# Kernel optimization log

Measured on AMD Instinct MI355X. Metric: run time of the kernel, lower is better.

Reference implementation:

```python
import jax, jax.numpy as jnp
import numpy as np

TOP_K = 2
TEMP = 1.0  # router_temperature
B, L, D, F, DF, DR, DH, E = 32, 256, 256, 8, 64, 256, 512, 8
DIN = D + DF  # expert/router input: concat(hidden, feat_emb)


def setup_inputs() -> dict:
    key = jax.random.key(0)
    ks = jax.random.split(key, 12)
    gn = lambda k, shape, fan: jax.random.normal(k, shape, dtype=jnp.float32) * (fan ** -0.5)
    return {
        "hidden": jax.random.normal(ks[0], (B, L, D), dtype=jnp.float32),
        "feat": jax.random.uniform(ks[1], (B, L, F), dtype=jnp.float32),
        "W_feat": gn(ks[2], (F, DF), F),
        "b_feat": jnp.zeros((DF,), jnp.float32),
        "Wr1": gn(ks[3], (DIN, DR), DIN),
        "br1": jnp.zeros((DR,), jnp.float32),
        "Wr2": gn(ks[4], (DR, E), DR),
        "br2": jnp.zeros((E,), jnp.float32),
        "We1": gn(ks[5], (E, DIN, DH), DIN),
        "be1": jnp.zeros((E, DH), jnp.float32),
        "We2": gn(ks[6], (E, DH, D), DH),
        "be2": jnp.zeros((E, D), jnp.float32),
    }


def reference(hidden, feat, W_feat, b_feat, Wr1, br1, Wr2, br2, We1, be1, We2, be2):
    # feature embedding
    feat_emb = feat @ W_feat + b_feat                       # [B,L,DF]
    x = jnp.concatenate([hidden, feat_emb], axis=-1)        # [B,L,DIN]

    # token-level learned router with temperature + top-k gating
    hr = jax.nn.gelu(x @ Wr1 + br1)                         # [B,L,DR]
    gate_logits = (hr @ Wr2 + br2) / TEMP                   # [B,L,E]
    topv, topi = jax.lax.top_k(gate_logits, TOP_K)          # [B,L,K]
    w = jax.nn.softmax(topv, axis=-1)                       # renormalized over top-k
    gate_weights = (jax.nn.one_hot(topi, E, dtype=w.dtype) * w[..., None]).sum(-2)  # [B,L,E]

    # experts: per-expert 2-layer MLP (dense compute, sparse combine via gates)
    he = jax.nn.gelu(jnp.einsum('bli,eih->bleh', x, We1) + be1)   # [B,L,E,DH]
    eo = jnp.einsum('bleh,eho->bleo', he, We2) + be2              # [B,L,E,D]
    stage_delta = jnp.einsum('ble,bleo->blo', gate_weights, eo)   # next_hidden - hidden

    return stage_delta, gate_weights, gate_logits
```

## Files before the change

### kernel.cpp

```cpp
#include <hip/hip_runtime.h>
#include <hip/hip_bf16.h>

#define N_TOK   8192
#define DMODEL  256
#define NFEAT   8
#define DFEAT   64
#define DIN     320
#define DRTR    256
#define NE      8
#define DH      512
#define TE      32
#define RTB     32
#define FIXCAP  128
#define FIXTHR  2e-3f

#define OUT_GATEW  (N_TOK*DMODEL)
#define OUT_LOGITS (N_TOK*DMODEL + N_TOK*NE)

typedef short v8s __attribute__((ext_vector_type(8)));
typedef float v4f __attribute__((ext_vector_type(4)));

__device__ __forceinline__ unsigned short f2bf(float f){
  unsigned u = __float_as_uint(f);
  return (unsigned short)((u + 0x7FFFu + ((u>>16)&1u)) >> 16);
}
__device__ __forceinline__ float bf2f(unsigned short h){
  return __uint_as_float(((unsigned)h)<<16);
}
__device__ __forceinline__ float gelu_tanh(float v){
  float u = 0.7978845608028654f * (v + 0.044715f * v * v * v);
  float a = fabsf(u);
  float e = __expf(-2.0f * a);
  float t = (1.0f - e) / (1.0f + e);
  t = copysignf(t, u);
  return 0.5f * v * (1.0f + t);
}

__global__ void k_init(int* __restrict__ cnts, int* __restrict__ nfix){
  if (threadIdx.x < NE) cnts[threadIdx.x] = 0;
  if (threadIdx.x == NE) *nfix = 0;
}

__global__ __launch_bounds__(256) void k_prep1(const float* __restrict__ W,
                                               unsigned short* __restrict__ dh,
                                               unsigned short* __restrict__ dl){
  int gid = blockIdx.x*256 + threadIdx.x;
  int l = gid & 63; int w = gid >> 6;
  int nt = w & 31; w >>= 5; int kstep = w % 10; int e = w / 10;
  int n = nt*16 + (l&15);
  int kb = kstep*32 + ((l>>4)<<3);
  const float* src = W + ((size_t)e*DIN + kb)*DH + n;
  unsigned short hs[8], ls[8];
  #pragma unroll
  for (int i=0;i<8;i++){
    float v = src[(size_t)i*DH];
    unsigned short h = f2bf(v);
    hs[i] = h; ls[i] = f2bf(v - bf2f(h));
  }
  size_t off = (size_t)gid*8;
  *(v8s*)(dh+off) = *(v8s*)hs;
  *(v8s*)(dl+off) = *(v8s*)ls;
}

__global__ __launch_bounds__(256) void k_prep2(const float* __restrict__ W,
                                               unsigned short* __restrict__ dh,
                                               unsigned short* __restrict__ dl){
  int gid = blockIdx.x*256 + threadIdx.x;
  int l = gid & 63; int w = gid >> 6;
  int nt = w & 15; w >>= 4; int kstep = w & 15; int e = w >> 4;
  int n = nt*16 + (l&15);
  int kb = kstep*32 + ((l>>4)<<3);
  const float* src = W + ((size_t)e*DH + kb)*DMODEL + n;
  unsigned short hs[8], ls[8];
  #pragma unroll
  for (int i=0;i<8;i++){
    float v = src[(size_t)i*DMODEL];
    unsigned short h = f2bf(v);
    hs[i] = h; ls[i] = f2bf(v - bf2f(h));
  }
  size_t off = (size_t)gid*8;
  *(v8s*)(dh+off) = *(v8s*)hs;
  *(v8s*)(dl+off) = *(v8s*)ls;
}

__global__ __launch_bounds__(256) void k_prepr(const float* __restrict__ W,
                                               unsigned short* __restrict__ dh,
                                               unsigned short* __restrict__ dl){
  int gid = blockIdx.x*256 + threadIdx.x;
  if (gid >= 10240) return;
  int l = gid & 63; int w = gid >> 6;
  int nt = w & 15; int kstep = w >> 4;
  int n = nt*16 + (l&15);
  int kb = kstep*32 + ((l>>4)<<3);
  const float* src = W + (size_t)kb*DRTR + n;
  unsigned short hs[8], ls[8];
  #pragma unroll
  for (int i=0;i<8;i++){
    float v = src[(size_t)i*DRTR];
    unsigned short h = f2bf(v);
    hs[i] = h; ls[i] = f2bf(v - bf2f(h));
  }
  size_t off = (size_t)gid*8;
  *(v8s*)(dh+off) = *(v8s*)hs;
  *(v8s*)(dl+off) = *(v8s*)ls;
}

#define MM6(c0,c1,ah0,ah1,al0,al1,bh,bl) do{ \
  c0 = __builtin_amdgcn_mfma_f32_16x16x32_bf16(ah0, bh, c0, 0,0,0); \
  c1 = __builtin_amdgcn_mfma_f32_16x16x32_bf16(ah1, bh, c1, 0,0,0); \
  c0 = __builtin_amdgcn_mfma_f32_16x16x32_bf16(al0, bh, c0, 0,0,0); \
  c1 = __builtin_amdgcn_mfma_f32_16x16x32_bf16(al1, bh, c1, 0,0,0); \
  c0 = __builtin_amdgcn_mfma_f32_16x16x32_bf16(ah0, bl, c0, 0,0,0); \
  c1 = __builtin_amdgcn_mfma_f32_16x16x32_bf16(ah1, bl, c1, 0,0,0); }while(0)

#define XLOFF  10496
#define HELOFF 16640

__global__ __launch_bounds__(512) void k_rmfma(
    const float* __restrict__ hidden, const float* __restrict__ feat,
    const float* __restrict__ Wf, const float* __restrict__ bfe,
    const unsigned short* __restrict__ Wr1h, const unsigned short* __restrict__ Wr1l,
    const float* __restrict__ br1,
    const float* __restrict__ Wr2, const float* __restrict__ br2,
    float* __restrict__ out,
    int* __restrict__ cnts, unsigned* __restrict__ lists, float* __restrict__ topw,
    int* __restrict__ nfix, int* __restrict__ fixlist)
{
  __shared__ unsigned short sm[21248];
  __shared__ float part_lds[512];
  __shared__ float lg_lds[RTB*NE];
  float* hrf = (float*)sm;
  const int tid = threadIdx.x;
  const int t0 = blockIdx.x * RTB;

  {
    float4 z = make_float4(0.f,0.f,0.f,0.f);
    float4* dst = ((float4*)out) + (size_t)blockIdx.x*2048 + tid;
    #pragma unroll
    for (int r=0;r<4;r++) dst[r*512] = z;
  }
  #pragma unroll
  for (int r=0;r<4;r++){
    int idx = r*512 + tid; int t = idx >> 6, lane = idx & 63;
    float4 h4 = ((const float4*)(hidden + (size_t)(t0+t)*DMODEL))[lane];
    unsigned short h0=f2bf(h4.x),h1=f2bf(h4.y),h2=f2bf(h4.z),h3=f2bf(h4.w);
    unsigned short l0=f2bf(h4.x-bf2f(h0)),l1=f2bf(h4.y-bf2f(h1)),
                   l2=f2bf(h4.z-bf2f(h2)),l3=f2bf(h4.w-bf2f(h3));
    uint2 hp, lp;
    hp.x=(unsigned)h0|((unsigned)h1<<16); hp.y=(unsigned)h2|((unsigned)h3<<16);
    lp.x=(unsigned)l0|((unsigned)l1<<16); lp.y=(unsigned)l2|((unsigned)l3<<16);
    *(uint2*)&sm[t*328 + lane*4]         = hp;
    *(uint2*)&sm[XLOFF + t*328 + lane*4] = lp;
  }
  #pragma unroll
  for (int r=0;r<4;r++){
    int idx = r*512 + tid; int t = idx >> 6, j = idx & 63;
    float acc = bfe[j];
    #pragma unroll
    for (int f=0; f<NFEAT; f++) acc += feat[(size_t)(t0+t)*NFEAT + f] * Wf[f*DFEAT + j];
    unsigned short h = f2bf(acc);
    sm[t*328 + DMODEL + j]         = h;
    sm[XLOFF + t*328 + DMODEL + j] = f2bf(acc - bf2f(h));
  }
  __syncthreads();

  const int wv = tid >> 6;
  const int l  = tid & 63;
  const int lg = l >> 4;
  const int lr = l & 15;

  v4f acc[2][2];
  {
    v4f z = {0.f,0.f,0.f,0.f};
    acc[0][0]=z; acc[0][1]=z; acc[1][0]=z; acc[1][1]=z;
    v8s bh_a[2], bl_a[2], bh_b[2], bl_b[2];
    auto ldBr = [&](int ks, v8s (&bh)[2], v8s (&bl)[2]){
      #pragma unroll
      for (int j=0;j<2;++j){
        size_t boff = ((size_t)(ks*16 + wv*2 + j)*64 + l)*8;
        bh[j] = *(const v8s*)(Wr1h + boff);
        bl[j] = *(const v8s*)(Wr1l + boff);
      }
    };
    ldBr(0, bh_a, bl_a);
    for (int ks=0; ks<10; ks+=2){
      v8s ah0 = *(const v8s*)&sm[( 0+lr)*328 + ks*32 + lg*8];
      v8s ah1 = *(const v8s*)&sm[(16+lr)*328 + ks*32 + lg*8];
      v8s al0 = *(const v8s*)&sm[XLOFF + ( 0+lr)*328 + ks*32 + lg*8];
      v8s al1 = *(const v8s*)&sm[XLOFF + (16+lr)*328 + ks*32 + lg*8];
      ldBr(ks+1, bh_b, bl_b);
      #pragma unroll
      for (int j=0;j<2;++j) MM6(acc[0][j],acc[1][j], ah0,ah1,al0,al1, bh_a[j],bl_a[j]);
      v8s ch0 = *(const v8s*)&sm[( 0+lr)*328 + (ks+1)*32 + lg*8];
      v8s ch1 = *(const v8s*)&sm[(16+lr)*328 + (ks+1)*32 + lg*8];
      v8s cl0 = *(const v8s*)&sm[XLOFF + ( 0+lr)*328 + (ks+1)*32 + lg*8];
      v8s cl1 = *(const v8s*)&sm[XLOFF + (16+lr)*328 + (ks+1)*32 + lg*8];
      if (ks+2<10) ldBr(ks+2, bh_a, bl_a);
      #pragma unroll
      for (int j=0;j<2;++j) MM6(acc[0][j],acc[1][j], ch0,ch1,cl0,cl1, bh_b[j],bl_b[j]);
    }
  }
  __syncthreads();
  #pragma unroll
  for (int j=0;j<2;++j){
    int col = (wv*2+j)*16 + lr;
    float b1 = br1[col];
    #pragma unroll
    for (int m=0;m<2;m++)
      #pragma unroll
      for (int r=0;r<4;r++){
        int row = m*16 + lg*4 + r;
        hrf[row*264 + col] = gelu_tanh(acc[m][j][r] + b1);
      }
  }
  __syncthreads();
  {
    int q = tid >> 8, rr = tid & 255, t = rr >> 3, e = rr & 7;
    float a0=0.f,a1=0.f,a2=0.f,a3=0.f;
    #pragma unroll 4
    for (int k4=0;k4<32;k4++){
      float4 h4 = ((const float4*)hrf)[t*66 + q*32 + k4];
      int row = q*128 + k4*4;
      a0 += h4.x * Wr2[(row+0)*NE + e];
      a1 += h4.y * Wr2[(row+1)*NE + e];
      a2 += h4.z * Wr2[(row+2)*NE + e];
      a3 += h4.w * Wr2[(row+3)*NE + e];
    }
    part_lds[tid] = (a0+a1)+(a2+a3);
  }
  __syncthreads();
  if (tid < RTB*NE){
    int t = tid >> 3, e = tid & 7;
    float lgv = br2[e] + part_lds[tid] + part_lds[tid+256];
    out[OUT_LOGITS + (size_t)(t0+t)*NE + e] = lgv;
    lg_lds[t*NE + e] = lgv;
  }
  __syncthreads();
  if (tid < RTB){
    int t = tid, tok = t0 + t;
    float v1=-3.4e38f, v2=-3.4e38f, v3=-3.4e38f; int i1=-1, i2=-1;
    #pragma unroll
    for (int e=0;e<NE;e++){
      float v = lg_lds[t*NE+e];
      if (v > v1){ v3=v2; v2=v1; i2=i1; v1=v; i1=e; }
      else if (v > v2){ v3=v2; v2=v; i2=e; }
      else if (v > v3){ v3=v; }
    }
    bool defer = false;
    if (v2 - v3 < FIXTHR){
      int fi = atomicAdd(nfix, 1);
      if (fi < FIXCAP){ fixlist[fi] = tok; defer = true; }
    }
    if (!defer){
      float d   = expf(v2 - v1);
      float inv = 1.0f/(1.0f + d);
      float w1 = inv, w2 = d*inv;
      #pragma unroll
      for (int e=0;e<NE;e++){
        float gv = (e==i1) ? w1 : ((e==i2) ? w2 : 0.f);
        out[OUT_GATEW + (size_t)tok*NE + e] = gv;
      }
      int p1 = atomicAdd(&cnts[i1], 1);
      lists[i1*N_TOK + p1] = (unsigned)(tok<<1);
      int p2 = atomicAdd(&cnts[i2], 1);
      lists[i2*N_TOK + p2] = (unsigned)((tok<<1) | 1);
      topw[tok*2]   = w1;
      topw[tok*2+1] = w2;
    }
  }
}

__global__ __launch_bounds__(256) void k_fix(
    const float* __restrict__ hidden, const float* __restrict__ feat,
    const float* __restrict__ Wf, const float* __restrict__ bfe,
    const float* __restrict__ Wr1, const float* __restrict__ br1,
    const float* __restrict__ Wr2, const float* __restrict__ br2,
    float* __restrict__ out, const int* __restrict__ nfix, const int* __restrict__ fixlist)
{
  int nf = *nfix; if (nf > FIXCAP) nf = FIXCAP;
  if ((int)blockIdx.x >= nf) return;
  const int tok = fixlist[blockIdx.x];
  const int tid = threadIdx.x;
  __shared__ float xf[DIN];
  __shared__ float hr[DRTR];
  if (tid < DMODEL) xf[tid] = hidden[(size_t)tok*DMODEL + tid];
  if (tid < DFEAT){
    float acc = bfe[tid];
    #pragma unroll
    for (int f=0; f<NFEAT; f++) acc += feat[(size_t)tok*NFEAT + f] * Wf[f*DFEAT + tid];
    xf[DMODEL + tid] = acc;
  }
  __syncthreads();
  {
    float acc = br1[tid];
    for (int i=0;i<DIN;i++) acc += xf[i] * Wr1[(size_t)i*DRTR + tid];
    hr[tid] = gelu_tanh(acc);
  }
  __syncthreads();
  if (tid < NE){
    float acc = br2[tid];
    for (int i=0;i<DRTR;i++) acc += hr[i] * Wr2[i*NE + tid];
    out[OUT_LOGITS + (size_t)tok*NE + tid] = acc;
  }
}

__global__ void k_gatefix(float* __restrict__ out,
                          int* __restrict__ cnts, unsigned* __restrict__ lists,
                          float* __restrict__ topw,
                          const int* __restrict__ nfix, const int* __restrict__ fixlist)
{
  int nf = *nfix; if (nf > FIXCAP) nf = FIXCAP;
  int i = threadIdx.x;
  if (i >= nf) return;
  int tok = fixlist[i];
  float v1=-3.4e38f, v2=-3.4e38f; int i1=-1, i2=-1;
  #pragma unroll
  for (int e=0;e<NE;e++){
    float v = out[OUT_LOGITS + (size_t)tok*NE + e];
    if (v > v1){ v2=v1; i2=i1; v1=v; i1=e; }
    else if (v > v2){ v2=v; i2=e; }
  }
  float d   = expf(v2 - v1);
  float inv = 1.0f/(1.0f + d);
  float w1 = inv, w2 = d*inv;
  #pragma unroll
  for (int e=0;e<NE;e++){
    float gv = (e==i1) ? w1 : ((e==i2) ? w2 : 0.f);
    out[OUT_GATEW + (size_t)tok*NE + e] = gv;
  }
  int p1 = atomicAdd(&cnts[i1], 1);
  lists[i1*N_TOK + p1] = (unsigned)(tok<<1);
  int p2 = atomicAdd(&cnts[i2], 1);
  lists[i2*N_TOK + p2] = (unsigned)((tok<<1) | 1);
  topw[tok*2]   = w1;
  topw[tok*2+1] = w2;
}

__global__ __launch_bounds__(512) void k_expert(
    const float* __restrict__ hidden, const float* __restrict__ feat,
    const float* __restrict__ Wf, const float* __restrict__ bfe,
    const int* __restrict__ cnts, const unsigned* __restrict__ lists,
    const float* __restrict__ topw,
    const unsigned short* __restrict__ W1h, const unsigned short* __restrict__ W1l,
    const unsigned short* __restrict__ W2h, const unsigned short* __restrict__ W2l,
    const float* __restrict__ be1, const float* __restrict__ be2,
    float* __restrict__ out)
{
  __shared__ unsigned short sm[33280];
  __shared__ int   tok_lds[TE];
  __shared__ float w_lds[TE];

  const int e    = blockIdx.x & 7;
  const int tile = blockIdx.x >> 3;
  const int cnt  = cnts[e];
  const int start = tile * TE;
  if (start >= cnt) return;
  const int ntk = min(TE, cnt - start);
  const int tid = threadIdx.x;

  if (tid < TE){
    if (tid < ntk){
      unsigned ent = lists[e*N_TOK + start + tid];
      int tok = (int)(ent >> 1);
      tok_lds[tid] = tok;
      w_lds[tid]   = topw[tok*2 + (ent & 1)];
    } else { tok_lds[tid] = -1; w_lds[tid] = 0.f; }
  }
  __syncthreads();
  #pragma unroll
  for (int r=0;r<4;r++){
    int idx = r*512 + tid; int t = idx >> 6, lane = idx & 63;
    int tok = tok_lds[t];
    float4 h4 = make_float4(0.f,0.f,0.f,0.f);
    if (tok >= 0) h4 = ((const float4*)(hidden + (size_t)tok*DMODEL))[lane];
    unsigned short h0=f2bf(h4.x),h1=f2bf(h4.y),h2=f2bf(h4.z),h3=f2bf(h4.w);
    unsigned short l0=f2bf(h4.x-bf2f(h0)),l1=f2bf(h4.y-bf2f(h1)),
                   l2=f2bf(h4.z-bf2f(h2)),l3=f2bf(h4.w-bf2f(h3));
    uint2 hp, lp;
    hp.x=(unsigned)h0|((unsigned)h1<<16); hp.y=(unsigned)h2|((unsigned)h3<<16);
    lp.x=(unsigned)l0|((unsigned)l1<<16); lp.y=(unsigned)l2|((unsigned)l3<<16);
    *(uint2*)&sm[t*328 + lane*4]         = hp;
    *(uint2*)&sm[XLOFF + t*328 + lane*4] = lp;
  }
  #pragma unroll
  for (int r=0;r<4;r++){
    int idx = r*512 + tid; int t = idx >> 6, j = idx & 63;
    int tok = tok_lds[t];
    float acc = 0.f;
    if (tok >= 0){
      acc = bfe[j];
      #pragma unroll
      for (int f=0; f<NFEAT; f++) acc += feat[(size_t)tok*NFEAT + f] * Wf[f*DFEAT + j];
    }
    unsigned short h = f2bf(acc);
    sm[t*328 + DMODEL + j]         = h;
    sm[XLOFF + t*328 + DMODEL + j] = f2bf(acc - bf2f(h));
  }
  __syncthreads();

  const int wv = tid >> 6;
  const int l  = tid & 63;
  const int lg = l >> 4;
  const int lr = l & 15;

  v4f acc1[2][4];
  {
    v4f z = {0.f,0.f,0.f,0.f};
    #pragma unroll
    for (int m=0;m<2;m++)
      #pragma unroll
      for (int j=0;j<4;j++) acc1[m][j] = z;
    const unsigned short* p1h = W1h + (size_t)e*163840;
    const unsigned short* p1l = W1l + (size_t)e*163840;
    auto ldB1 = [&](int ks, int jh, v8s (&bh)[2], v8s (&bl)[2]){
      #pragma unroll
      for (int j=0;j<2;++j){
        size_t boff = ((size_t)(ks*32 + wv*4 + jh*2 + j)*64 + l)*8;
        bh[j] = *(const v8s*)(p1h + boff);
        bl[j] = *(const v8s*)(p1l + boff);
      }
    };
    v8s bh_a[2], bl_a[2], bh_b[2], bl_b[2];
    ldB1(0,0,bh_a,bl_a);
    for (int ks=0; ks<10; ++ks){
      v8s ah0 = *(const v8s*)&sm[( 0+lr)*328 + ks*32 + lg*8];
      v8s ah1 = *(const v8s*)&sm[(16+lr)*328 + ks*32 + lg*8];
      v8s al0 = *(const v8s*)&sm[XLOFF + ( 0+lr)*328 + ks*32 + lg*8];
      v8s al1 = *(const v8s*)&sm[XLOFF + (16+lr)*328 + ks*32 + lg*8];
      ldB1(ks,1,bh_b,bl_b);
      #pragma unroll
      for (int j=0;j<2;++j) MM6(acc1[0][j],acc1[1][j], ah0,ah1,al0,al1, bh_a[j],bl_a[j]);
      if (ks<9) ldB1(ks+1,0,bh_a,bl_a);
      #pragma unroll
      for (int j=0;j<2;++j) MM6(acc1[0][2+j],acc1[1][2+j], ah0,ah1,al0,al1, bh_b[j],bl_b[j]);
    }
  }
  __syncthreads();
  #pragma unroll
  for (int j=0;j<4;++j){
    int col = (wv*4+j)*16 + lr;
    float b1 = be1[e*DH + col];
    #pragma unroll
    for (int m=0;m<2;m++)
      #pragma unroll
      for (int r=0;r<4;r++){
        float v = gelu_tanh(acc1[m][j][r] + b1);
        int row = m*16 + lg*4 + r;
        unsigned short h = f2bf(v);
        sm[row*520 + col]          = h;
        sm[HELOFF + row*520 + col] = f2bf(v - bf2f(h));
      }
  }
  __syncthreads();
  v4f acc2[2][2];
  {
    v4f z = {0.f,0.f,0.f,0.f};
    acc2[0][0]=z; acc2[0][1]=z; acc2[1][0]=z; acc2[1][1]=z;
    const unsigned short* p2h = W2h + (size_t)e*131072;
    const unsigned short* p2l = W2l + (size_t)e*131072;
    auto ldB2 = [&](int ks, v8s (&bh)[2], v8s (&bl)[2]){
      #pragma unroll
      for (int j=0;j<2;++j){
        size_t boff = ((size_t)(ks*16 + wv*2 + j)*64 + l)*8;
        bh[j] = *(const v8s*)(p2h + boff);
        bl[j] = *(const v8s*)(p2l + boff);
      }
    };
    v8s bh_a[2], bl_a[2], bh_b[2], bl_b[2];
    ldB2(0,bh_a,bl_a);
    for (int ks=0; ks<16; ks+=2){
      v8s ah0 = *(const v8s*)&sm[( 0+lr)*520 + ks*32 + lg*8];
      v8s ah1 = *(const v8s*)&sm[(16+lr)*520 + ks*32 + lg*8];
      v8s al0 = *(const v8s*)&sm[HELOFF + ( 0+lr)*520 + ks*32 + lg*8];
      v8s al1 = *(const v8s*)&sm[HELOFF + (16+lr)*520 + ks*32 + lg*8];
      ldB2(ks+1, bh_b, bl_b);
      #pragma unroll
      for (int j=0;j<2;++j) MM6(acc2[0][j],acc2[1][j], ah0,ah1,al0,al1, bh_a[j],bl_a[j]);
      v8s ch0 = *(const v8s*)&sm[( 0+lr)*520 + (ks+1)*32 + lg*8];
      v8s ch1 = *(const v8s*)&sm[(16+lr)*520 + (ks+1)*32 + lg*8];
      v8s cl0 = *(const v8s*)&sm[HELOFF + ( 0+lr)*520 + (ks+1)*32 + lg*8];
      v8s cl1 = *(const v8s*)&sm[HELOFF + (16+lr)*520 + (ks+1)*32 + lg*8];
      if (ks+2<16) ldB2(ks+2, bh_a, bl_a);
      #pragma unroll
      for (int j=0;j<2;++j) MM6(acc2[0][j],acc2[1][j], ch0,ch1,cl0,cl1, bh_b[j],bl_b[j]);
    }
  }
  #pragma unroll
  for (int j=0;j<2;++j){
    int col = (wv*2+j)*16 + lr;
    float b2 = be2[e*DMODEL + col];
    #pragma unroll
    for (int m=0;m<2;m++)
      #pragma unroll
      for (int r=0;r<4;r++){
        int row = m*16 + lg*4 + r;
        if (row < ntk){
          float w = w_lds[row];
          atomicAdd(out + (size_t)tok_lds[row]*DMODEL + col,
                    w*(acc2[m][j][r] + b2));
        }
      }
  }
}

extern "C" void kernel_launch(void* const* d_in, const int* in_sizes, int n_in,
                              void* d_out, int out_size, void* d_ws, size_t ws_size,
                              hipStream_t stream)
{
  (void)in_sizes; (void)n_in; (void)out_size; (void)ws_size;
  const float* hidden = (const float*)d_in[0];
  const float* feat   = (const float*)d_in[1];
  const float* Wf     = (const float*)d_in[2];
  const float* bfe    = (const float*)d_in[3];
  const float* Wr1    = (const float*)d_in[4];
  const float* br1    = (const float*)d_in[5];
  const float* Wr2    = (const float*)d_in[6];
  const float* br2    = (const float*)d_in[7];
  const float* We1    = (const float*)d_in[8];
  const float* be1    = (const float*)d_in[9];
  const float* We2    = (const float*)d_in[10];
  const float* be2    = (const float*)d_in[11];
  float* out = (float*)d_out;

  char* ws = (char*)d_ws;
  int*      cnts    = (int*)ws;
  int*      nfix    = (int*)(ws + 64);
  int*      fixlist = (int*)(ws + 128);
  unsigned* lists   = (unsigned*)(ws + 1024);
  float*    topw    = (float*)(ws + 263168);
  unsigned short* W1h  = (unsigned short*)(ws + 328704);
  unsigned short* W1l  = (unsigned short*)(ws + 2950144);
  unsigned short* W2h  = (unsigned short*)(ws + 5571584);
  unsigned short* W2l  = (unsigned short*)(ws + 7668736);
  unsigned short* Wr1h = (unsigned short*)(ws + 9765888);
  unsigned short* Wr1l = (unsigned short*)(ws + 9929728);

  hipLaunchKernelGGL(k_init, dim3(1), dim3(64), 0, stream, cnts, nfix);
  hipLaunchKernelGGL(k_prep1, dim3(640), dim3(256), 0, stream, We1, W1h, W1l);
  hipLaunchKernelGGL(k_prep2, dim3(512), dim3(256), 0, stream, We2, W2h, W2l);
  hipLaunchKernelGGL(k_prepr, dim3(40),  dim3(256), 0, stream, Wr1, Wr1h, Wr1l);
  hipLaunchKernelGGL(k_rmfma, dim3(N_TOK/RTB), dim3(512), 0, stream,
                     hidden, feat, Wf, bfe, Wr1h, Wr1l, br1, Wr2, br2,
                     out, cnts, lists, topw, nfix, fixlist);
  hipLaunchKernelGGL(k_fix, dim3(FIXCAP), dim3(256), 0, stream,
                     hidden, feat, Wf, bfe, Wr1, br1, Wr2, br2, out, nfix, fixlist);
  hipLaunchKernelGGL(k_gatefix, dim3(1), dim3(FIXCAP), 0, stream,
                     out, cnts, lists, topw, nfix, fixlist);
  hipLaunchKernelGGL(k_expert, dim3((N_TOK/TE)*NE), dim3(512), 0, stream,
                     hidden, feat, Wf, bfe, cnts, lists, topw,
                     W1h, W1l, W2h, W2l, be1, be2, out);
}
```

Before: 293.8 us.

## Fuse weight prep kernels, stage through LDS, use fragment-ordered LDS layout in experts

Merges the init kernel and the three weight-split prep kernels into one launch. Each block now loads a contiguous weight tile into LDS with coalesced float4 reads before writing the hi/lo bf16 fragments. The expert kernel stores activations and the GELU hidden layer in LDS directly in MFMA fragment order, so A-operand reads become contiguous and need no padding. It also issues the first weight prefetches earlier and adds sched_barriers to pin the order of loads and MFMAs. The cost is more complex index math, and the scheduling barriers may keep the compiler from interleaving instructions well.

```diff
diff --git a/kernel.cpp b/kernel.cpp
--- a/kernel.cpp
+++ b/kernel.cpp
@@ -36,73 +36,84 @@
   return 0.5f * v * (1.0f + t);
 }
 
-__global__ void k_init(int* __restrict__ cnts, int* __restrict__ nfix){
-  if (threadIdx.x < NE) cnts[threadIdx.x] = 0;
-  if (threadIdx.x == NE) *nfix = 0;
-}
-
-__global__ __launch_bounds__(256) void k_prep1(const float* __restrict__ W,
-                                               unsigned short* __restrict__ dh,
-                                               unsigned short* __restrict__ dl){
-  int gid = blockIdx.x*256 + threadIdx.x;
-  int l = gid & 63; int w = gid >> 6;
-  int nt = w & 31; w >>= 5; int kstep = w % 10; int e = w / 10;
-  int n = nt*16 + (l&15);
-  int kb = kstep*32 + ((l>>4)<<3);
-  const float* src = W + ((size_t)e*DIN + kb)*DH + n;
-  unsigned short hs[8], ls[8];
-  #pragma unroll
-  for (int i=0;i<8;i++){
-    float v = src[(size_t)i*DH];
-    unsigned short h = f2bf(v);
-    hs[i] = h; ls[i] = f2bf(v - bf2f(h));
-  }
-  size_t off = (size_t)gid*8;
-  *(v8s*)(dh+off) = *(v8s*)hs;
-  *(v8s*)(dl+off) = *(v8s*)ls;
-}
-
-__global__ __launch_bounds__(256) void k_prep2(const float* __restrict__ W,
-                                               unsigned short* __restrict__ dh,
-                                               unsigned short* __restrict__ dl){
-  int gid = blockIdx.x*256 + threadIdx.x;
-  int l = gid & 63; int w = gid >> 6;
-  int nt = w & 15; w >>= 4; int kstep = w & 15; int e = w >> 4;
-  int n = nt*16 + (l&15);
-  int kb = kstep*32 + ((l>>4)<<3);
-  const float* src = W + ((size_t)e*DH + kb)*DMODEL + n;
-  unsigned short hs[8], ls[8];
-  #pragma unroll
-  for (int i=0;i<8;i++){
-    float v = src[(size_t)i*DMODEL];
-    unsigned short h = f2bf(v);
-    hs[i] = h; ls[i] = f2bf(v - bf2f(h));
-  }
-  size_t off = (size_t)gid*8;
-  *(v8s*)(dh+off) = *(v8s*)hs;
-  *(v8s*)(dl+off) = *(v8s*)ls;
-}
-
-__global__ __launch_bounds__(256) void k_prepr(const float* __restrict__ W,
-                                               unsigned short* __restrict__ dh,
-                                               unsigned short* __restrict__ dl){
-  int gid = blockIdx.x*256 + threadIdx.x;
-  if (gid >= 10240) return;
-  int l = gid & 63; int w = gid >> 6;
-  int nt = w & 15; int kstep = w >> 4;
-  int n = nt*16 + (l&15);
-  int kb = kstep*32 + ((l>>4)<<3);
-  const float* src = W + (size_t)kb*DRTR + n;
-  unsigned short hs[8], ls[8];
-  #pragma unroll
-  for (int i=0;i<8;i++){
-    float v = src[(size_t)i*DRTR];
-    unsigned short h = f2bf(v);
-    hs[i] = h; ls[i] = f2bf(v - bf2f(h));
-  }
-  size_t off = (size_t)gid*8;
-  *(v8s*)(dh+off) = *(v8s*)hs;
-  *(v8s*)(dl+off) = *(v8s*)ls;
+__global__ __launch_bounds__(256) void k_prep(
+    const float* __restrict__ We1, const float* __restrict__ We2,
+    const float* __restrict__ Wr1,
+    unsigned short* __restrict__ W1h, unsigned short* __restrict__ W1l,
+    unsigned short* __restrict__ W2h, unsigned short* __restrict__ W2l,
+    unsigned short* __restrict__ Wr1h, unsigned short* __restrict__ Wr1l,
+    int* __restrict__ cnts, int* __restrict__ nfix)
+{
+  __shared__ float lds[16384];
+  const int b = blockIdx.x;
+  const int tid = threadIdx.x;
+  if (b < 80){
+    int e = b/10, kstep = b%10;
+    const float* src = We1 + ((size_t)e*DIN + kstep*32)*DH;
+    #pragma unroll
+    for (int r=0;r<16;r++) ((float4*)lds)[r*256+tid] = ((const float4*)src)[r*256+tid];
+    __syncthreads();
+    #pragma unroll
+    for (int r=0;r<8;r++){
+      int ent = r*256+tid; int nt = ent>>6, l = ent&63;
+      int n = nt*16 + (l&15); int k0 = (l>>4)*8;
+      unsigned short hs[8], ls[8];
+      #pragma unroll
+      for (int i=0;i<8;i++){
+        float v = lds[(k0+i)*DH + n];
+        unsigned short h = f2bf(v);
+        hs[i]=h; ls[i]=f2bf(v - bf2f(h));
+      }
+      size_t gid = ((size_t)(e*10+kstep)*32 + nt)*64 + l;
+      *(v8s*)(W1h+gid*8) = *(v8s*)hs;
+      *(v8s*)(W1l+gid*8) = *(v8s*)ls;
+    }
+  } else if (b < 208){
+    int e = (b-80)/16, kstep = (b-80)%16;
+    const float* src = We2 + ((size_t)e*DH + kstep*32)*DMODEL;
+    #pragma unroll
+    for (int r=0;r<8;r++) ((float4*)lds)[r*256+tid] = ((const float4*)src)[r*256+tid];
+    __syncthreads();
+    #pragma unroll
+    for (int r=0;r<4;r++){
+      int ent = r*256+tid; int nt = ent>>6, l = ent&63;
+      int n = nt*16 + (l&15); int k0 = (l>>4)*8;
+      unsigned short hs[8], ls[8];
+      #pragma unroll
+      for (int i=0;i<8;i++){
+        float v = lds[(k0+i)*DMODEL + n];
+        unsigned short h = f2bf(v);
+        hs[i]=h; ls[i]=f2bf(v - bf2f(h));
+      }
+      size_t gid = ((size_t)(e*16+kstep)*16 + nt)*64 + l;
+      *(v8s*)(W2h+gid*8) = *(v8s*)hs;
+      *(v8s*)(W2l+gid*8) = *(v8s*)ls;
+    }
+  } else if (b < 218){
+    int kstep = b-208;
+    const float* src = Wr1 + (size_t)kstep*32*DRTR;
+    #pragma unroll
+    for (int r=0;r<8;r++) ((float4*)lds)[r*256+tid] = ((const float4*)src)[r*256+tid];
+    __syncthreads();
+    #pragma unroll
+    for (int r=0;r<4;r++){
+      int ent = r*256+tid; int nt = ent>>6, l = ent&63;
+      int n = nt*16 + (l&15); int k0 = (l>>4)*8;
+      unsigned short hs[8], ls[8];
+      #pragma unroll
+      for (int i=0;i<8;i++){
+        float v = lds[(k0+i)*DRTR + n];
+        unsigned short h = f2bf(v);
+        hs[i]=h; ls[i]=f2bf(v - bf2f(h));
+      }
+      size_t gid = ((size_t)kstep*16 + nt)*64 + l;
+      *(v8s*)(Wr1h+gid*8) = *(v8s*)hs;
+      *(v8s*)(Wr1l+gid*8) = *(v8s*)ls;
+    }
+  } else {
+    if (tid < NE) cnts[tid] = 0;
+    if (tid == NE) *nfix = 0;
+  }
 }
 
 #define MM6(c0,c1,ah0,ah1,al0,al1,bh,bl) do{ \
@@ -114,7 +125,6 @@
   c1 = __builtin_amdgcn_mfma_f32_16x16x32_bf16(ah1, bl, c1, 0,0,0); }while(0)
 
 #define XLOFF  10496
-#define HELOFF 16640
 
 __global__ __launch_bounds__(512) void k_rmfma(
     const float* __restrict__ hidden, const float* __restrict__ feat,
@@ -189,6 +199,7 @@
       v8s al0 = *(const v8s*)&sm[XLOFF + ( 0+lr)*328 + ks*32 + lg*8];
       v8s al1 = *(const v8s*)&sm[XLOFF + (16+lr)*328 + ks*32 + lg*8];
       ldBr(ks+1, bh_b, bl_b);
+      __builtin_amdgcn_sched_barrier(0);
       #pragma unroll
       for (int j=0;j<2;++j) MM6(acc[0][j],acc[1][j], ah0,ah1,al0,al1, bh_a[j],bl_a[j]);
       v8s ch0 = *(const v8s*)&sm[( 0+lr)*328 + (ks+1)*32 + lg*8];
@@ -196,6 +207,7 @@
       v8s cl0 = *(const v8s*)&sm[XLOFF + ( 0+lr)*328 + (ks+1)*32 + lg*8];
       v8s cl1 = *(const v8s*)&sm[XLOFF + (16+lr)*328 + (ks+1)*32 + lg*8];
       if (ks+2<10) ldBr(ks+2, bh_a, bl_a);
+      __builtin_amdgcn_sched_barrier(0);
       #pragma unroll
       for (int j=0;j<2;++j) MM6(acc[0][j],acc[1][j], ch0,ch1,cl0,cl1, bh_b[j],bl_b[j]);
     }
@@ -336,6 +348,8 @@
   topw[tok*2+1] = w2;
 }
 
+#define XFL  10240
+#define HFL  16384
 __global__ __launch_bounds__(512) void k_expert(
     const float* __restrict__ hidden, const float* __restrict__ feat,
     const float* __restrict__ Wf, const float* __restrict__ bfe,
@@ -346,7 +360,7 @@
     const float* __restrict__ be1, const float* __restrict__ be2,
     float* __restrict__ out)
 {
-  __shared__ unsigned short sm[33280];
+  __shared__ unsigned short sm[32768];
   __shared__ int   tok_lds[TE];
   __shared__ float w_lds[TE];
 
@@ -357,6 +371,24 @@
   if (start >= cnt) return;
   const int ntk = min(TE, cnt - start);
   const int tid = threadIdx.x;
+  const int wv = tid >> 6;
+  const int l  = tid & 63;
+  const int lg = l >> 4;
+  const int lr = l & 15;
+
+  const unsigned short* p1h = W1h + (size_t)e*163840;
+  const unsigned short* p1l = W1l + (size_t)e*163840;
+
+  v8s bh_a[2], bl_a[2], bh_b[2], bl_b[2];
+  auto ldB1 = [&](int ks, int jh, v8s (&bh)[2], v8s (&bl)[2]){
+    #pragma unroll
+    for (int j=0;j<2;++j){
+      size_t boff = ((size_t)(ks*32 + wv*4 + jh*2 + j)*64 + l)*8;
+      bh[j] = *(const v8s*)(p1h + boff);
+      bl[j] = *(const v8s*)(p1l + boff);
+    }
+  };
+  ldB1(0,0,bh_a,bl_a);
 
   if (tid < TE){
     if (tid < ntk){
@@ -368,40 +400,44 @@
   }
   __syncthreads();
   #pragma unroll
-  for (int r=0;r<4;r++){
-    int idx = r*512 + tid; int t = idx >> 6, lane = idx & 63;
-    int tok = tok_lds[t];
-    float4 h4 = make_float4(0.f,0.f,0.f,0.f);
-    if (tok >= 0) h4 = ((const float4*)(hidden + (size_t)tok*DMODEL))[lane];
-    unsigned short h0=f2bf(h4.x),h1=f2bf(h4.y),h2=f2bf(h4.z),h3=f2bf(h4.w);
-    unsigned short l0=f2bf(h4.x-bf2f(h0)),l1=f2bf(h4.y-bf2f(h1)),
-                   l2=f2bf(h4.z-bf2f(h2)),l3=f2bf(h4.w-bf2f(h3));
-    uint2 hp, lp;
-    hp.x=(unsigned)h0|((unsigned)h1<<16); hp.y=(unsigned)h2|((unsigned)h3<<16);
-    lp.x=(unsigned)l0|((unsigned)l1<<16); lp.y=(unsigned)l2|((unsigned)l3<<16);
-    *(uint2*)&sm[t*328 + lane*4]         = hp;
-    *(uint2*)&sm[XLOFF + t*328 + lane*4] = lp;
-  }
-  #pragma unroll
-  for (int r=0;r<4;r++){
-    int idx = r*512 + tid; int t = idx >> 6, j = idx & 63;
-    int tok = tok_lds[t];
-    float acc = 0.f;
-    if (tok >= 0){
-      acc = bfe[j];
-      #pragma unroll
-      for (int f=0; f<NFEAT; f++) acc += feat[(size_t)tok*NFEAT + f] * Wf[f*DFEAT + j];
-    }
-    unsigned short h = f2bf(acc);
-    sm[t*328 + DMODEL + j]         = h;
-    sm[XLOFF + t*328 + DMODEL + j] = f2bf(acc - bf2f(h));
-  }
-  __syncthreads();
-
-  const int wv = tid >> 6;
-  const int l  = tid & 63;
-  const int lg = l >> 4;
-  const int lr = l & 15;
+  for (int r=0;r<3;r++){
+    int idx = r*512 + tid;
+    if (idx < 1280){
+      int le = idx & 63; int rest = idx >> 6;
+      int m = rest & 1, ks = rest >> 1;
+      int t = m*16 + (le & 15);
+      int kb = ks*32 + (le >> 4)*8;
+      int tok = tok_lds[t];
+      float v[8];
+      if (tok < 0){
+        #pragma unroll
+        for (int i=0;i<8;i++) v[i] = 0.f;
+      } else if (kb < DMODEL){
+        float4 a = *(const float4*)(hidden + (size_t)tok*DMODEL + kb);
+        float4 b = *(const float4*)(hidden + (size_t)tok*DMODEL + kb + 4);
+        v[0]=a.x; v[1]=a.y; v[2]=a.z; v[3]=a.w;
+        v[4]=b.x; v[5]=b.y; v[6]=b.z; v[7]=b.w;
+      } else {
+        int j0 = kb - DMODEL;
+        #pragma unroll
+        for (int i=0;i<8;i++){
+          float acc = bfe[j0+i];
+          #pragma unroll
+          for (int f=0; f<NFEAT; f++) acc += feat[(size_t)tok*NFEAT + f] * Wf[f*DFEAT + j0+i];
+          v[i] = acc;
+        }
+      }
+      unsigned short hs[8], ls[8];
+      #pragma unroll
+      for (int i=0;i<8;i++){
+        unsigned short h = f2bf(v[i]);
+        hs[i]=h; ls[i]=f2bf(v[i]-bf2f(h));
+      }
+      *(v8s*)&sm[idx*8]       = *(v8s*)hs;
+      *(v8s*)&sm[XFL + idx*8] = *(v8s*)ls;
+    }
+  }
+  __syncthreads();
 
   v4f acc1[2][4];
   {
@@ -410,45 +446,51 @@
     for (int m=0;m<2;m++)
       #pragma unroll
       for (int j=0;j<4;j++) acc1[m][j] = z;
-    const unsigned short* p1h = W1h + (size_t)e*163840;
-    const unsigned short* p1l = W1l + (size_t)e*163840;
-    auto ldB1 = [&](int ks, int jh, v8s (&bh)[2], v8s (&bl)[2]){
-      #pragma unroll
-      for (int j=0;j<2;++j){
-        size_t boff = ((size_t)(ks*32 + wv*4 + jh*2 + j)*64 + l)*8;
-        bh[j] = *(const v8s*)(p1h + boff);
-        bl[j] = *(const v8s*)(p1l + boff);
-      }
-    };
-    v8s bh_a[2], bl_a[2], bh_b[2], bl_b[2];
-    ldB1(0,0,bh_a,bl_a);
     for (int ks=0; ks<10; ++ks){
-      v8s ah0 = *(const v8s*)&sm[( 0+lr)*328 + ks*32 + lg*8];
-      v8s ah1 = *(const v8s*)&sm[(16+lr)*328 + ks*32 + lg*8];
-      v8s al0 = *(const v8s*)&sm[XLOFF + ( 0+lr)*328 + ks*32 + lg*8];
-      v8s al1 = *(const v8s*)&sm[XLOFF + (16+lr)*328 + ks*32 + lg*8];
+      v8s ah0 = *(const v8s*)&sm[((ks*2+0)*64 + l)*8];
+      v8s ah1 = *(const v8s*)&sm[((ks*2+1)*64 + l)*8];
+      v8s al0 = *(const v8s*)&sm[XFL + ((ks*2+0)*64 + l)*8];
+      v8s al1 = *(const v8s*)&sm[XFL + ((ks*2+1)*64 + l)*8];
       ldB1(ks,1,bh_b,bl_b);
+      __builtin_amdgcn_sched_barrier(0);
       #pragma unroll
       for (int j=0;j<2;++j) MM6(acc1[0][j],acc1[1][j], ah0,ah1,al0,al1, bh_a[j],bl_a[j]);
       if (ks<9) ldB1(ks+1,0,bh_a,bl_a);
+      __builtin_amdgcn_sched_barrier(0);
       #pragma unroll
       for (int j=0;j<2;++j) MM6(acc1[0][2+j],acc1[1][2+j], ah0,ah1,al0,al1, bh_b[j],bl_b[j]);
     }
   }
+  const unsigned short* p2h = W2h + (size_t)e*131072;
+  const unsigned short* p2l = W2l + (size_t)e*131072;
+  v8s ch_a[2], cl_a[2], ch_b[2], cl_b[2];
+  auto ldB2 = [&](int ks, v8s (&bh)[2], v8s (&bl)[2]){
+    #pragma unroll
+    for (int j=0;j<2;++j){
+      size_t boff = ((size_t)(ks*16 + wv*2 + j)*64 + l)*8;
+      bh[j] = *(const v8s*)(p2h + boff);
+      bl[j] = *(const v8s*)(p2l + boff);
+    }
+  };
+  ldB2(0, ch_a, cl_a);
   __syncthreads();
   #pragma unroll
   for (int j=0;j<4;++j){
-    int col = (wv*4+j)*16 + lr;
+    int W = wv*4 + j;
+    int col = W*16 + lr;
     float b1 = be1[e*DH + col];
+    int ks2 = W >> 1;
+    int lg2 = (W*2 + (lr>>3)) & 3;
+    int i   = lr & 7;
     #pragma unroll
     for (int m=0;m<2;m++)
       #pragma unroll
       for (int r=0;r<4;r++){
         float v = gelu_tanh(acc1[m][j][r] + b1);
-        int row = m*16 + lg*4 + r;
         unsigned short h = f2bf(v);
-        sm[row*520 + col]          = h;
-        sm[HELOFF + row*520 + col] = f2bf(v - bf2f(h));
+        int dst = ((ks2*2 + m)*64 + lg2*16 + lg*4 + r)*8 + i;
+        sm[dst]       = h;
+        sm[HFL + dst] = f2bf(v - bf2f(h));
       }
   }
   __syncthreads();
@@ -456,33 +498,23 @@
   {
     v4f z = {0.f,0.f,0.f,0.f};
     acc2[0][0]=z; acc2[0][1]=z; acc2[1][0]=z; acc2[1][1]=z;
-    const unsigned short* p2h = W2h + (size_t)e*131072;
-    const unsigned short* p2l = W2l + (size_t)e*131072;
-    auto ldB2 = [&](int ks, v8s (&bh)[2], v8s (&bl)[2]){
-      #pragma unroll
-      for (int j=0;j<2;++j){
-        size_t boff = ((size_t)(ks*16 + wv*2 + j)*64 + l)*8;
-        bh[j] = *(const v8s*)(p2h + boff);
-        bl[j] = *(const v8s*)(p2l + boff);
-      }
-    };
-    v8s bh_a[2], bl_a[2], bh_b[2], bl_b[2];
-    ldB2(0,bh_a,bl_a);
     for (int ks=0; ks<16; ks+=2){
-      v8s ah0 = *(const v8s*)&sm[( 0+lr)*520 + ks*32 + lg*8];
-      v8s ah1 = *(const v8s*)&sm[(16+lr)*520 + ks*32 + lg*8];
-      v8s al0 = *(const v8s*)&sm[HELOFF + ( 0+lr)*520 + ks*32 + lg*8];
-      v8s al1 = *(const v8s*)&sm[HELOFF + (16+lr)*520 + ks*32 + lg*8];
-      ldB2(ks+1, bh_b, bl_b);
-      #pragma unroll
-      for (int j=0;j<2;++j) MM6(acc2[0][j],acc2[1][j], ah0,ah1,al0,al1, bh_a[j],bl_a[j]);
-      v8s ch0 = *(const v8s*)&sm[( 0+lr)*520 + (ks+1)*32 + lg*8];
-      v8s ch1 = *(const v8s*)&sm[(16+lr)*520 + (ks+1)*32 + lg*8];
-      v8s cl0 = *(const v8s*)&sm[HELOFF + ( 0+lr)*520 + (ks+1)*32 + lg*8];
-      v8s cl1 = *(const v8s*)&sm[HELOFF + (16+lr)*520 + (ks+1)*32 + lg*8];
-      if (ks+2<16) ldB2(ks+2, bh_a, bl_a);
-      #pragma unroll
-      for (int j=0;j<2;++j) MM6(acc2[0][j],acc2[1][j], ch0,ch1,cl0,cl1, bh_b[j],bl_b[j]);
+      v8s ah0 = *(const v8s*)&sm[((ks*2+0)*64 + l)*8];
+      v8s ah1 = *(const v8s*)&sm[((ks*2+1)*64 + l)*8];
+      v8s al0 = *(const v8s*)&sm[HFL + ((ks*2+0)*64 + l)*8];
+      v8s al1 = *(const v8s*)&sm[HFL + ((ks*2+1)*64 + l)*8];
+      ldB2(ks+1, ch_b, cl_b);
+      __builtin_amdgcn_sched_barrier(0);
+      #pragma unroll
+      for (int j=0;j<2;++j) MM6(acc2[0][j],acc2[1][j], ah0,ah1,al0,al1, ch_a[j],cl_a[j]);
+      v8s dh0 = *(const v8s*)&sm[(((ks+1)*2+0)*64 + l)*8];
+      v8s dh1 = *(const v8s*)&sm[(((ks+1)*2+1)*64 + l)*8];
+      v8s dl0 = *(const v8s*)&sm[HFL + (((ks+1)*2+0)*64 + l)*8];
+      v8s dl1 = *(const v8s*)&sm[HFL + (((ks+1)*2+1)*64 + l)*8];
+      if (ks+2<16) ldB2(ks+2, ch_a, cl_a);
+      __builtin_amdgcn_sched_barrier(0);
+      #pragma unroll
+      for (int j=0;j<2;++j) MM6(acc2[0][j],acc2[1][j], dh0,dh1,dl0,dl1, ch_b[j],cl_b[j]);
     }
   }
   #pragma unroll
@@ -535,10 +567,8 @@
   unsigned short* Wr1h = (unsigned short*)(ws + 9765888);
   unsigned short* Wr1l = (unsigned short*)(ws + 9929728);
 
-  hipLaunchKernelGGL(k_init, dim3(1), dim3(64), 0, stream, cnts, nfix);
-  hipLaunchKernelGGL(k_prep1, dim3(640), dim3(256), 0, stream, We1, W1h, W1l);
-  hipLaunchKernelGGL(k_prep2, dim3(512), dim3(256), 0, stream, We2, W2h, W2l);
-  hipLaunchKernelGGL(k_prepr, dim3(40),  dim3(256), 0, stream, Wr1, Wr1h, Wr1l);
+  hipLaunchKernelGGL(k_prep, dim3(219), dim3(256), 0, stream,
+                     We1, We2, Wr1, W1h, W1l, W2h, W2l, Wr1h, Wr1l, cnts, nfix);
   hipLaunchKernelGGL(k_rmfma, dim3(N_TOK/RTB), dim3(512), 0, stream,
                      hidden, feat, Wf, bfe, Wr1h, Wr1l, br1, Wr2, br2,
                      out, cnts, lists, topw, nfix, fixlist);
```

Result: slower. 310.3 us (+5.6%).
